# Kernel tuning notes

Measured on AMD Instinct MI355X. Metric: run time of the kernel, lower is better.

## Reference

```python
import jax, jax.numpy as jnp
import numpy as np


def _tri(x):
    # triangle wave, period=0.1, amplitude=1:
    # (a/p) * (p - |x % (2p) - p| - p/2) = 10 * (0.05 - |x % 0.2 - 0.1|)
    return 10.0 * (0.05 - jnp.abs(jnp.mod(x, 0.2) - 0.1))


def _cdist(a, b):
    # pairwise Euclidean distance between rows of a [n, d] and b [m, d]
    d2 = jnp.sum((a[:, None, :] - b[None, :, :]) ** 2, axis=-1)
    return jnp.sqrt(jnp.maximum(d2, 0.0))


def setup_inputs() -> dict:
    key = jax.random.key(0)
    ks = jax.random.split(key, 8)
    B, L, D = 131072, 256, 20
    x = jax.random.normal(ks[0], (B, L), dtype=jnp.float32)
    # layer_params ~ U(-1, 1) of shape [l, dimensions]
    p0, p1, p2, p3 = (jax.random.uniform(ks[1 + i], (L, D), dtype=jnp.float32,
                                         minval=-1.0, maxval=1.0) for i in range(4))
    # layer_biases ~ U(-0.1, 0.1) of shape [l, 1]; bias[0] is never used in forward
    b1, b2, b3 = (jax.random.uniform(ks[5 + i], (L, 1), dtype=jnp.float32,
                                     minval=-0.1, maxval=0.1) for i in range(3))
    return {"x": x, "p0": p0, "p1": p1, "p2": p2, "p3": p3,
            "b1": b1, "b2": b2, "b3": b3}


def reference(x, p0, p1, p2, p3, b1, b2, b3):
    params = [p0, p1, p2, p3]
    biases = [None, b1, b2, b3]  # forward only uses biases[i+1]
    n = len(params)
    z = x
    for i in range(n - 1):
        scale = 1.0 / np.sqrt(params[i].shape[0]).astype(np.float32)
        W = _tri(_cdist(params[i], params[i + 1])) * scale  # [l_i, l_{i+1}]
        z = z @ W + biases[i + 1].T                          # [B, l_{i+1}]
        if i < n - 2:
            z = jax.nn.relu(z)
    return z
```

## Files before the change

kernel.cpp:

```cpp
#include <hip/hip_runtime.h>
#include <hip/hip_bf16.h>
#include <hip/hip_fp16.h>

typedef _Float16 half8 __attribute__((ext_vector_type(8)));
typedef _Float16 half4 __attribute__((ext_vector_type(4)));
typedef float    floatx4 __attribute__((ext_vector_type(4)));

#define BM 64

__global__ void make_weights_frag(const float* __restrict__ p0, const float* __restrict__ p1,
                                  const float* __restrict__ p2, const float* __restrict__ p3,
                                  _Float16* __restrict__ wt) {
    int idx  = blockIdx.x * blockDim.x + threadIdx.x;
    int lane = idx & 63;
    int nf   = (idx >> 6) & 3;
    int s    = (idx >> 8) & 7;
    int wc   = (idx >> 11) & 3;
    int l    = idx >> 13;
    int n  = wc * 64 + nf * 16 + (lane & 15);
    int k0 = s * 32 + (lane >> 4) * 8;
    const float* P[4] = {p0, p1, p2, p3};
    const float* pb = P[l + 1] + n * 20;
    float pbr[20];
    #pragma unroll
    for (int i = 0; i < 20; ++i) pbr[i] = pb[i];
    half8 o;
    #pragma unroll
    for (int j = 0; j < 8; ++j) {
        const float* pa = P[l] + (k0 + j) * 20;
        float d2 = 0.f;
        #pragma unroll
        for (int i = 0; i < 20; ++i) { float df = pa[i] - pbr[i]; d2 += df * df; }
        float d = sqrtf(d2);
        float m = fmodf(d, 0.2f);
        o[j] = (_Float16)(10.0f * (0.05f - fabsf(m - 0.1f)) * 0.0625f);
    }
    *reinterpret_cast<half8*>(wt + (size_t)idx * 8) = o;
}

__global__ __launch_bounds__(512, 4) void pcn_fused(
    const float* __restrict__ x, const _Float16* __restrict__ wt,
    const float* __restrict__ b1, const float* __restrict__ b2,
    const float* __restrict__ b3, float* __restrict__ out) {

    __shared__ __align__(16) _Float16 zlds[2][BM * 256];

    const int t    = threadIdx.x;
    const int lane = t & 63;
    const int wv   = t >> 6;
    const int l15  = lane & 15;
    const int lg   = lane >> 4;
    const size_t row0 = (size_t)blockIdx.x * BM;

    char* const zb0 = reinterpret_cast<char*>(&zlds[0][0]);
    char* const zb1 = reinterpret_cast<char*>(&zlds[1][0]);

    half8   bb[3][2];
    floatx4 acc[4][2];

    auto wfrag = [&](int g, int j) -> const half8* {
        const int gl = g >> 3, gs = g & 7;
        return reinterpret_cast<const half8*>(
            wt + (((size_t)gl * 4 + (wv >> 1)) << 14) + gs * 2048
               + ((wv & 1) * 2 + j) * 512 + lane * 8);
    };

    {
        floatx4 xr[8];
        #pragma unroll
        for (int i = 0; i < 8; ++i) {
            int g   = i * 512 + t;
            int row = g >> 6, c4 = g & 63;
            xr[i] = *reinterpret_cast<const floatx4*>(x + (row0 + row) * 256 + c4 * 4);
        }
        #pragma unroll
        for (int i = 0; i < 8; ++i) {
            int g   = i * 512 + t;
            int row = g >> 6, c4 = g & 63;
            half4 h;
            h[0] = (_Float16)xr[i][0]; h[1] = (_Float16)xr[i][1];
            h[2] = (_Float16)xr[i][2]; h[3] = (_Float16)xr[i][3];
            int chunk = (c4 >> 1) ^ (row & 7);
            *reinterpret_cast<half4*>(zb0 + row * 512 + chunk * 16 + (c4 & 1) * 8) = h;
        }
    }
    #pragma unroll
    for (int j = 0; j < 2; ++j) bb[0][j] = *wfrag(0, j);
    #pragma unroll
    for (int j = 0; j < 2; ++j) bb[1][j] = *wfrag(1, j);
    __syncthreads();

    #pragma unroll
    for (int l = 0; l < 3; ++l) {
        const float* bias = (l == 0) ? b1 : (l == 1) ? b2 : b3;
        char* const rz = (l == 1) ? zb1 : zb0;

        #pragma unroll
        for (int j = 0; j < 2; ++j) {
            const float bv = bias[wv * 32 + j * 16 + l15];
            #pragma unroll
            for (int mf = 0; mf < 4; ++mf)
                acc[mf][j] = floatx4{bv, bv, bv, bv};
        }

        #pragma unroll
        for (int s = 0; s < 8; ++s) {
            const int g = l * 8 + s;
            if (g + 2 < 24) {
                #pragma unroll
                for (int j = 0; j < 2; ++j)
                    bb[(g + 2) % 3][j] = *wfrag(g + 2, j);
            }
            const int vchunk = (s * 4 + lg) ^ (l15 & 7);
            half8 a[4];
            #pragma unroll
            for (int mf = 0; mf < 4; ++mf)
                a[mf] = *reinterpret_cast<const half8*>(
                    rz + (mf * 16 + l15) * 512 + vchunk * 16);
            #pragma unroll
            for (int mf = 0; mf < 4; ++mf)
                #pragma unroll
                for (int j = 0; j < 2; ++j)
                    acc[mf][j] = __builtin_amdgcn_mfma_f32_16x16x32_f16(
                        a[mf], bb[g % 3][j], acc[mf][j], 0, 0, 0);
        }

        if (l < 2) {
            char* const wz = (l == 0) ? zb1 : zb0;
            #pragma unroll
            for (int j = 0; j < 2; ++j) {
                const int n = wv * 32 + j * 16 + l15;
                #pragma unroll
                for (int mf = 0; mf < 4; ++mf) {
                    const int mrow = mf * 16 + lg * 4;
                    #pragma unroll
                    for (int r = 0; r < 4; ++r) {
                        float v = fmaxf(acc[mf][j][r], 0.0f);
                        const int row  = mrow + r;
                        const int byte = row * 512 + (((n >> 3) ^ (row & 7)) << 4)
                                       + (n & 7) * 2;
                        *reinterpret_cast<_Float16*>(wz + byte) = (_Float16)v;
                    }
                }
            }
            __syncthreads();
        } else {
            #pragma unroll
            for (int j = 0; j < 2; ++j) {
                const int n = wv * 32 + j * 16 + l15;
                #pragma unroll
                for (int mf = 0; mf < 4; ++mf) {
                    const size_t mrow = row0 + mf * 16 + lg * 4;
                    #pragma unroll
                    for (int r = 0; r < 4; ++r)
                        out[(mrow + r) * 256 + n] = acc[mf][j][r];
                }
            }
        }
    }
}

extern "C" void kernel_launch(void* const* d_in, const int* in_sizes, int n_in,
                              void* d_out, int out_size, void* d_ws, size_t ws_size,
                              hipStream_t stream) {
    const float* x  = (const float*)d_in[0];
    const float* p0 = (const float*)d_in[1];
    const float* p1 = (const float*)d_in[2];
    const float* p2 = (const float*)d_in[3];
    const float* p3 = (const float*)d_in[4];
    const float* b1 = (const float*)d_in[5];
    const float* b2 = (const float*)d_in[6];
    const float* b3 = (const float*)d_in[7];
    float* out = (float*)d_out;
    _Float16* wt = (_Float16*)d_ws;

    const int B = in_sizes[0] / 256;

    make_weights_frag<<<96, 256, 0, stream>>>(p0, p1, p2, p3, wt);
    pcn_fused<<<B / BM, 512, 0, stream>>>(x, wt, b1, b2, b3, out);
}
```

Baseline: 84.67 us.

## Make fused MLP kernel persistent over four tiles with next-tile x prefetch

Each block now processes four 64-row tiles instead of one, alternating the two LDS buffers. During the third layer of each tile it loads the next tile's x rows from global memory and writes them into the free buffer, and it reloads the first weight fragments for the next tile. The aim is to hide global load latency behind MFMA work and amortise block startup. In exchange the grid is four times smaller, which cuts the parallelism available across CUs, and the extra xr registers may lower occupancy. The loop hardcodes TPB/2 == 2 through the it2==1 check.

```diff
diff --git a/kernel.cpp b/kernel.cpp
--- a/kernel.cpp
+++ b/kernel.cpp
@@ -6,7 +6,8 @@
 typedef _Float16 half4 __attribute__((ext_vector_type(4)));
 typedef float    floatx4 __attribute__((ext_vector_type(4)));
 
-#define BM 64
+#define BM  64
+#define TPB 4
 
 __global__ void make_weights_frag(const float* __restrict__ p0, const float* __restrict__ p1,
                                   const float* __restrict__ p2, const float* __restrict__ p3,
@@ -50,13 +51,13 @@
     const int wv   = t >> 6;
     const int l15  = lane & 15;
     const int lg   = lane >> 4;
-    const size_t row0 = (size_t)blockIdx.x * BM;
 
     char* const zb0 = reinterpret_cast<char*>(&zlds[0][0]);
     char* const zb1 = reinterpret_cast<char*>(&zlds[1][0]);
 
     half8   bb[3][2];
     floatx4 acc[4][2];
+    floatx4 xr[4];
 
     auto wfrag = [&](int g, int j) -> const half8* {
         const int gl = g >> 3, gs = g & 7;
@@ -65,98 +66,127 @@
                + ((wv & 1) * 2 + j) * 512 + lane * 8);
     };
 
-    {
-        floatx4 xr[8];
-        #pragma unroll
-        for (int i = 0; i < 8; ++i) {
-            int g   = i * 512 + t;
+    auto xload_batch = [&](size_t r0, int b) {
+        #pragma unroll
+        for (int i = 0; i < 4; ++i) {
+            int g   = (b * 4 + i) * 512 + t;
             int row = g >> 6, c4 = g & 63;
-            xr[i] = *reinterpret_cast<const floatx4*>(x + (row0 + row) * 256 + c4 * 4);
-        }
-        #pragma unroll
-        for (int i = 0; i < 8; ++i) {
-            int g   = i * 512 + t;
+            xr[i] = *reinterpret_cast<const floatx4*>(x + (r0 + row) * 256 + c4 * 4);
+        }
+    };
+    auto xwrite_batch = [&](char* zb, int b) {
+        #pragma unroll
+        for (int i = 0; i < 4; ++i) {
+            int g   = (b * 4 + i) * 512 + t;
             int row = g >> 6, c4 = g & 63;
             half4 h;
             h[0] = (_Float16)xr[i][0]; h[1] = (_Float16)xr[i][1];
             h[2] = (_Float16)xr[i][2]; h[3] = (_Float16)xr[i][3];
             int chunk = (c4 >> 1) ^ (row & 7);
-            *reinterpret_cast<half4*>(zb0 + row * 512 + chunk * 16 + (c4 & 1) * 8) = h;
-        }
-    }
+            *reinterpret_cast<half4*>(zb + row * 512 + chunk * 16 + (c4 & 1) * 8) = h;
+        }
+    };
+
+    const size_t tile0 = (size_t)blockIdx.x * (TPB * BM);
+
+    xload_batch(tile0, 0); xwrite_batch(zb0, 0);
+    xload_batch(tile0, 1); xwrite_batch(zb0, 1);
     #pragma unroll
     for (int j = 0; j < 2; ++j) bb[0][j] = *wfrag(0, j);
     #pragma unroll
     for (int j = 0; j < 2; ++j) bb[1][j] = *wfrag(1, j);
     __syncthreads();
 
-    #pragma unroll
-    for (int l = 0; l < 3; ++l) {
-        const float* bias = (l == 0) ? b1 : (l == 1) ? b2 : b3;
-        char* const rz = (l == 1) ? zb1 : zb0;
-
-        #pragma unroll
-        for (int j = 0; j < 2; ++j) {
-            const float bv = bias[wv * 32 + j * 16 + l15];
-            #pragma unroll
-            for (int mf = 0; mf < 4; ++mf)
-                acc[mf][j] = floatx4{bv, bv, bv, bv};
-        }
-
-        #pragma unroll
-        for (int s = 0; s < 8; ++s) {
-            const int g = l * 8 + s;
-            if (g + 2 < 24) {
-                #pragma unroll
-                for (int j = 0; j < 2; ++j)
-                    bb[(g + 2) % 3][j] = *wfrag(g + 2, j);
-            }
-            const int vchunk = (s * 4 + lg) ^ (l15 & 7);
-            half8 a[4];
-            #pragma unroll
-            for (int mf = 0; mf < 4; ++mf)
-                a[mf] = *reinterpret_cast<const half8*>(
-                    rz + (mf * 16 + l15) * 512 + vchunk * 16);
-            #pragma unroll
-            for (int mf = 0; mf < 4; ++mf)
-                #pragma unroll
-                for (int j = 0; j < 2; ++j)
-                    acc[mf][j] = __builtin_amdgcn_mfma_f32_16x16x32_f16(
-                        a[mf], bb[g % 3][j], acc[mf][j], 0, 0, 0);
-        }
-
-        if (l < 2) {
-            char* const wz = (l == 0) ? zb1 : zb0;
+    auto do_tile = [&](size_t row0, char* bufX, char* bufY, bool pfx, bool last) {
+        #pragma unroll
+        for (int l = 0; l < 3; ++l) {
+            const float* bias = (l == 0) ? b1 : (l == 1) ? b2 : b3;
+            char* const rz = (l == 1) ? bufY : bufX;
+
             #pragma unroll
             for (int j = 0; j < 2; ++j) {
-                const int n = wv * 32 + j * 16 + l15;
-                #pragma unroll
-                for (int mf = 0; mf < 4; ++mf) {
-                    const int mrow = mf * 16 + lg * 4;
+                const float bv = bias[wv * 32 + j * 16 + l15];
+                #pragma unroll
+                for (int mf = 0; mf < 4; ++mf)
+                    acc[mf][j] = floatx4{bv, bv, bv, bv};
+            }
+
+            #pragma unroll
+            for (int s = 0; s < 8; ++s) {
+                const int g = l * 8 + s;
+                if (g + 2 < 24) {
                     #pragma unroll
-                    for (int r = 0; r < 4; ++r) {
-                        float v = fmaxf(acc[mf][j][r], 0.0f);
-                        const int row  = mrow + r;
-                        const int byte = row * 512 + (((n >> 3) ^ (row & 7)) << 4)
-                                       + (n & 7) * 2;
-                        *reinterpret_cast<_Float16*>(wz + byte) = (_Float16)v;
+                    for (int j = 0; j < 2; ++j)
+                        bb[(g + 2) % 3][j] = *wfrag(g + 2, j);
+                }
+                if (l == 2 && pfx) {
+                    if (s == 0) xload_batch(row0 + BM, 0);
+                    if (s == 3) xwrite_batch(bufY, 0);
+                    if (s == 4) xload_batch(row0 + BM, 1);
+                }
+                const int vchunk = (s * 4 + lg) ^ (l15 & 7);
+                half8 a[4];
+                #pragma unroll
+                for (int mf = 0; mf < 4; ++mf)
+                    a[mf] = *reinterpret_cast<const half8*>(
+                        rz + (mf * 16 + l15) * 512 + vchunk * 16);
+                #pragma unroll
+                for (int mf = 0; mf < 4; ++mf)
+                    #pragma unroll
+                    for (int j = 0; j < 2; ++j)
+                        acc[mf][j] = __builtin_amdgcn_mfma_f32_16x16x32_f16(
+                            a[mf], bb[g % 3][j], acc[mf][j], 0, 0, 0);
+            }
+
+            if (l < 2) {
+                char* const wz = (l == 0) ? bufY : bufX;
+                #pragma unroll
+                for (int j = 0; j < 2; ++j) {
+                    const int n = wv * 32 + j * 16 + l15;
+                    #pragma unroll
+                    for (int mf = 0; mf < 4; ++mf) {
+                        const int mrow = mf * 16 + lg * 4;
+                        #pragma unroll
+                        for (int r = 0; r < 4; ++r) {
+                            float v = fmaxf(acc[mf][j][r], 0.0f);
+                            const int row  = mrow + r;
+                            const int byte = row * 512 + (((n >> 3) ^ (row & 7)) << 4)
+                                           + (n & 7) * 2;
+                            *reinterpret_cast<_Float16*>(wz + byte) = (_Float16)v;
+                        }
                     }
                 }
-            }
-            __syncthreads();
-        } else {
-            #pragma unroll
-            for (int j = 0; j < 2; ++j) {
-                const int n = wv * 32 + j * 16 + l15;
-                #pragma unroll
-                for (int mf = 0; mf < 4; ++mf) {
-                    const size_t mrow = row0 + mf * 16 + lg * 4;
-                    #pragma unroll
-                    for (int r = 0; r < 4; ++r)
-                        out[(mrow + r) * 256 + n] = acc[mf][j][r];
-                }
-            }
-        }
+                __syncthreads();
+            }
+        }
+
+        if (pfx) {
+            xwrite_batch(bufY, 1);
+            #pragma unroll
+            for (int j = 0; j < 2; ++j) bb[0][j] = *wfrag(0, j);
+            #pragma unroll
+            for (int j = 0; j < 2; ++j) bb[1][j] = *wfrag(1, j);
+        }
+        if (!last) __syncthreads();
+
+        #pragma unroll
+        for (int j = 0; j < 2; ++j) {
+            const int n = wv * 32 + j * 16 + l15;
+            #pragma unroll
+            for (int mf = 0; mf < 4; ++mf) {
+                const size_t mrow = row0 + mf * 16 + lg * 4;
+                #pragma unroll
+                for (int r = 0; r < 4; ++r)
+                    out[(mrow + r) * 256 + n] = acc[mf][j][r];
+            }
+        }
+    };
+
+    #pragma unroll 1
+    for (int it2 = 0; it2 < TPB / 2; ++it2) {
+        const size_t rowA = tile0 + (size_t)it2 * (2 * BM);
+        do_tile(rowA,      zb0, zb1, true,      false);
+        do_tile(rowA + BM, zb1, zb0, it2 == 0,  it2 == 1);
     }
 }
 
@@ -177,5 +207,5 @@
     const int B = in_sizes[0] / 256;
 
     make_weights_frag<<<96, 256, 0, stream>>>(p0, p1, p2, p3, wt);
-    pcn_fused<<<B / BM, 512, 0, stream>>>(x, wt, b1, b2, b3, out);
+    pcn_fused<<<B / (BM * TPB), 512, 0, stream>>>(x, wt, b1, b2, b3, out);
 }
```

Result: slower. 326.5 us (+285.6%).
